# Kernel optimization log

Hardware: AMD Instinct MI355X
Metric: run time of the kernel (lower is better)

## Reference

```python
import jax, jax.numpy as jnp
import numpy as np

N_USERS = 100000
N_ITEMS = 50000
EMB_DIM = 64
N_EDGES = 1000000
N_HOPS = 3
EPS = 1e-12  # F.normalize default eps


def _l2_normalize(x):
    # F.normalize(x): x / max(||x||_2, eps) along dim=1
    norm = jnp.sqrt(jnp.sum(x * x, axis=1, keepdims=True))
    return x / jnp.maximum(norm, EPS)


def setup_inputs() -> dict:
    key = jax.random.key(0)
    k1, k2, k3, k4 = jax.random.split(key, 4)
    user_emb = jax.random.normal(k1, (N_USERS, EMB_DIM), dtype=jnp.float32)
    item_emb = jax.random.normal(k2, (N_ITEMS, EMB_DIM), dtype=jnp.float32)
    user_indices = jax.random.randint(k3, (N_EDGES,), 0, N_USERS, dtype=jnp.int32)
    item_indices = jax.random.randint(k4, (N_EDGES,), 0, N_ITEMS, dtype=jnp.int32)
    return {"user_emb": user_emb, "item_emb": item_emb,
            "user_indices": user_indices, "item_indices": item_indices}


def reference(user_emb, item_emb, user_indices, item_indices):
    # mess_dropout=False, node_dropout=False (deterministic reference)
    user_agg = user_emb
    item_agg = item_emb
    user_ui_emb = jnp.zeros_like(user_emb)
    item_ui_emb = jnp.zeros_like(item_emb)
    for _ in range(N_HOPS):
        # bipartite message passing: gather from opposite side, scatter_add to own side
        msg_to_users = item_agg[item_indices]            # [E, D]
        msg_to_items = user_agg[user_indices]            # [E, D]
        user_agg = jax.ops.segment_sum(msg_to_users, user_indices, num_segments=N_USERS)
        item_agg = jax.ops.segment_sum(msg_to_items, item_indices, num_segments=N_ITEMS)
        item_agg = _l2_normalize(item_agg)
        user_agg = _l2_normalize(user_agg)
        user_ui_emb = user_agg + user_ui_emb
        item_ui_emb = item_agg + item_ui_emb
    item_ui_emb = item_ui_emb + item_emb
    user_ui_emb = user_ui_emb + user_emb
    return (item_ui_emb, user_ui_emb)
```

## Files before the change

### kernel.cpp

```cpp
#include <hip/hip_runtime.h>

#define N_USERS 100000
#define N_ITEMS 50000
#define NROWS (N_USERS + N_ITEMS)
#define EMB 64
#define N_EDGES 1000000

#define SH_U 9
#define SH_I 8
#define NBUK 196
#define B1 256
#define CHUNK ((N_EDGES + B1 - 1) / B1)
#define HN (2 * NBUK * B1)
#define HTILE 4096
#define HTILES ((HN + HTILE - 1) / HTILE)
#define DBINS 64

typedef unsigned short u16;
typedef u16 us8 __attribute__((ext_vector_type(8)));
typedef u16 us4 __attribute__((ext_vector_type(4)));
typedef float f4 __attribute__((ext_vector_type(4)));

static __device__ __forceinline__ float bf2f(u16 h) {
    return __uint_as_float(((unsigned)h) << 16);
}
static __device__ __forceinline__ u16 f2bf(float f) {
    unsigned u = __float_as_uint(f);
    return (u16)((u + 0x7FFFu + ((u >> 16) & 1u)) >> 16);
}

static __device__ __forceinline__ int hphys(int L) {
    int sb = L >> 8;
    int blk = L & 255;
    return blk * (2 * NBUK) + sb;
}

__global__ void conv_kernel(const float* __restrict__ a, u16* __restrict__ b, int n4) {
    int t = blockIdx.x * blockDim.x + threadIdx.x;
    if (t >= n4) return;
    f4 v = ((const f4*)a)[t];
    us4 w;
    w.x = f2bf(v.x); w.y = f2bf(v.y); w.z = f2bf(v.z); w.w = f2bf(v.w);
    ((us4*)b)[t] = w;
}

__global__ void histA_kernel(const int* __restrict__ uidx, const int* __restrict__ iidx,
                             int* __restrict__ H) {
    __shared__ int hu[NBUK];
    __shared__ int hi[NBUK];
    int tid = threadIdx.x, blk = blockIdx.x;
    for (int b = tid; b < NBUK; b += 256) { hu[b] = 0; hi[b] = 0; }
    __syncthreads();
    int e0 = blk * CHUNK;
    int e1 = e0 + CHUNK; if (e1 > N_EDGES) e1 = N_EDGES;
    for (int e = e0 + tid; e < e1; e += 256) {
        atomicAdd(&hu[uidx[e] >> SH_U], 1);
        atomicAdd(&hi[iidx[e] >> SH_I], 1);
    }
    __syncthreads();
    int* Hb = H + blk * (2 * NBUK);
    for (int b = tid; b < NBUK; b += 256) {
        Hb[b] = hu[b];
        Hb[NBUK + b] = hi[b];
    }
}

__global__ void hscan_tile_kernel(const int* __restrict__ H, int* __restrict__ part) {
    int t = blockIdx.x, tid = threadIdx.x;
    int base = t * HTILE;
    int s = 0;
    for (int i = tid; i < HTILE; i += 256) {
        int L = base + i;
        if (L < HN) s += H[hphys(L)];
    }
    #pragma unroll
    for (int o = 32; o > 0; o >>= 1) s += __shfl_xor(s, o);
    __shared__ int wsum[4];
    if ((tid & 63) == 0) wsum[tid >> 6] = s;
    __syncthreads();
    if (tid == 0) part[t] = wsum[0] + wsum[1] + wsum[2] + wsum[3];
}

__global__ void hscan_write_kernel(const int* __restrict__ H, const int* __restrict__ part,
                                   int* __restrict__ HB) {
    int t = blockIdx.x, tid = threadIdx.x;
    int base = t * HTILE;

    __shared__ int lds[HTILE];
    for (int i = tid; i < HTILE; i += 256) {
        int L = base + i;
        lds[i] = (L < HN) ? H[hphys(L)] : 0;
    }
    __syncthreads();

    int pbase = 0;
    for (int p = 0; p < t; ++p) pbase += part[p];

    int tsum = 0;
    #pragma unroll
    for (int i = 0; i < 16; ++i) tsum += lds[tid * 16 + i];

    int lane = tid & 63, wid = tid >> 6;
    int x = tsum;
    #pragma unroll
    for (int o = 1; o < 64; o <<= 1) {
        int tt = __shfl_up(x, o);
        if (lane >= o) x += tt;
    }
    __shared__ int wsum[4];
    if (lane == 63) wsum[wid] = x;
    __syncthreads();
    int wbase = 0;
    for (int w = 0; w < wid; ++w) wbase += wsum[w];

    int run = pbase + wbase + x - tsum;
    #pragma unroll
    for (int i = 0; i < 16; ++i) {
        int L = base + tid * 16 + i;
        if (L < HN) HB[L] = run;
        run += lds[tid * 16 + i];
    }
}

__global__ void scatterA_kernel(const int* __restrict__ uidx, const int* __restrict__ iidx,
                                const int* __restrict__ HB, int* __restrict__ rec) {
    __shared__ int cu[NBUK];
    __shared__ int ci[NBUK];
    int tid = threadIdx.x, blk = blockIdx.x;
    for (int sb = tid; sb < 2 * NBUK; sb += 256) {
        int v = HB[sb * B1 + blk];
        if (sb < NBUK) cu[sb] = v; else ci[sb - NBUK] = v;
    }
    __syncthreads();
    int e0 = blk * CHUNK;
    int e1 = e0 + CHUNK; if (e1 > N_EDGES) e1 = N_EDGES;
    for (int e = e0 + tid; e < e1; e += 256) {
        int u = uidx[e];
        int i = iidx[e];
        int pu = atomicAdd(&cu[u >> SH_U], 1);
        rec[pu] = ((u & 511) << 16) | i;
        int pi = atomicAdd(&ci[i >> SH_I], 1);
        rec[pi] = ((i & 255) << 17) | u;
    }
}

__global__ void bucketB_kernel(const int* __restrict__ HB, const int* __restrict__ rec,
                               int* __restrict__ offs_u, int* __restrict__ offs_i,
                               int* __restrict__ list, int* __restrict__ perm) {
    int sb = blockIdx.x, tid = threadIdx.x;
    int side = (sb >= NBUK) ? 1 : 0;
    int b = sb - side * NBUK;
    int start = HB[sb * B1];
    int end = (sb == 2 * NBUK - 1) ? 2 * N_EDGES : HB[(sb + 1) * B1];
    int shift = side ? 17 : 16;
    int mask  = side ? 0x1FFFF : 0xFFFF;
    int nd    = side ? 256 : 512;
    int dbase = side ? (b << SH_I) : (b << SH_U);
    int n     = side ? N_ITEMS : N_USERS;
    int rel   = start - side * N_EDGES;
    int* offs = side ? offs_i : offs_u;

    __shared__ int cnt[512];
    __shared__ int scn[512];
    __shared__ int wsum[4];
    __shared__ int dh[DBINS];
    __shared__ int dsc[DBINS];
    if (tid < 256) { cnt[tid] = 0; cnt[256 + tid] = 0; }
    if (tid < DBINS) dh[tid] = 0;
    __syncthreads();

    for (int r = start + tid; r < end; r += 256)
        atomicAdd(&cnt[rec[r] >> shift], 1);
    __syncthreads();

    int a0 = cnt[2 * tid], a1 = cnt[2 * tid + 1];
    int s = a0 + a1;
    int lane = tid & 63, wid = tid >> 6;
    int x = s;
    #pragma unroll
    for (int o = 1; o < 64; o <<= 1) {
        int tt = __shfl_up(x, o);
        if (lane >= o) x += tt;
    }
    if (lane == 63) wsum[wid] = x;
    __syncthreads();
    int wbase = 0;
    for (int w = 0; w < wid; ++w) wbase += wsum[w];
    int excl = wbase + x - s;
    scn[2 * tid] = excl;
    scn[2 * tid + 1] = excl + a0;
    __syncthreads();

    for (int dl = tid; dl < nd; dl += 256) {
        int dg = dbase + dl;
        if (dg < n) offs[dg] = rel + scn[dl];
    }
    if (b == NBUK - 1 && tid == 0) offs[n] = (end - side * N_EDGES);
    __syncthreads();

    for (int r = start + tid; r < end; r += 256) {
        int v = rec[r];
        int dl = v >> shift;
        int pos = atomicAdd(&scn[dl], 1);
        list[start + pos] = (v & mask) << 7;
    }

    int nv = n - dbase; if (nv > nd) nv = nd;
    for (int dl = tid; dl < nv; dl += 256) {
        int d = cnt[dl]; if (d > DBINS - 1) d = DBINS - 1;
        atomicAdd(&dh[d], 1);
    }
    __syncthreads();
    if (tid < DBINS) {
        int v = dh[tid];
        int xx = v;
        #pragma unroll
        for (int o = 1; o < DBINS; o <<= 1) {
            int tt = __shfl_up(xx, o);
            if (tid >= o) xx += tt;
        }
        dsc[tid] = xx - v;
    }
    __syncthreads();
    if (tid < DBINS) dh[tid] = dsc[tid];
    __syncthreads();
    int pwbase = side ? (N_USERS + dbase) : dbase;
    for (int dl = tid; dl < nv; dl += 256) {
        int d = cnt[dl]; if (d > DBINS - 1) d = DBINS - 1;
        int p = atomicAdd(&dh[d], 1);
        perm[pwbase + p] = pwbase + dl;
    }
}

__global__ void gather_norm_v3(const u16* __restrict__ srcU,
                               const u16* __restrict__ srcI,
                               const int* __restrict__ offs_u, const int* __restrict__ list_u,
                               const int* __restrict__ offs_i, const int* __restrict__ list_i,
                               const int* __restrict__ perm,
                               u16* __restrict__ aggU, u16* __restrict__ aggI,
                               const u16* __restrict__ h0U, const u16* __restrict__ h0I,
                               const u16* __restrict__ h1U, const u16* __restrict__ h1I,
                               float* __restrict__ outU, float* __restrict__ outI,
                               const float* __restrict__ initU, const float* __restrict__ initI,
                               int final_hop) {
    int t = blockIdx.x * blockDim.x + threadIdx.x;
    int lane = t & 63;
    int grp = lane >> 3, sub = lane & 7;
    int slot = (t >> 6) * 8 + grp;

    int rid = (slot < NROWS) ? perm[slot] : -1;
    bool valid = rid >= 0;
    bool isU = valid && (rid < N_USERS);
    int rr = isU ? rid : rid - N_USERS;

    int beg = 0, deg = 0;
    if (valid) {
        const int* offs = isU ? offs_u : offs_i;
        beg = offs[rr];
        deg = offs[rr + 1] - beg;
    }
    const int* list = isU ? list_u : list_i;
    const u16* src  = isU ? srcU : srcI;
    const char* srcB = (const char*)src;
    unsigned suboff = (unsigned)(sub << 4);
    const int* lp = list + beg;

    int dmax = deg;
    dmax = max(dmax, __shfl_xor(dmax, 8));
    dmax = max(dmax, __shfl_xor(dmax, 16));
    dmax = max(dmax, __shfl_xor(dmax, 32));

    float acc[8] = {0.f, 0.f, 0.f, 0.f, 0.f, 0.f, 0.f, 0.f};

    #pragma unroll 8
    for (int e = 0; e < dmax; ++e) {
        if (e < deg) {
            unsigned jb = (unsigned)lp[e];
            us8 v = *(const us8*)(srcB + (jb + suboff));
            #pragma unroll
            for (int i = 0; i < 8; ++i) acc[i] += bf2f(v[i]);
        }
    }

    float q = 0.f;
    #pragma unroll
    for (int i = 0; i < 8; ++i) q += acc[i] * acc[i];
    q += __shfl_xor(q, 1);
    q += __shfl_xor(q, 2);
    q += __shfl_xor(q, 4);
    float inv = 1.f / fmaxf(sqrtf(q), 1e-12f);

    if (!valid) return;
    size_t ro = (size_t)rr * EMB + (sub << 3);

    if (!final_hop) {
        u16* agg = isU ? aggU : aggI;
        us8 w;
        #pragma unroll
        for (int i = 0; i < 8; ++i) w[i] = f2bf(acc[i] * inv);
        *(us8*)(agg + ro) = w;
    } else {
        const u16* h0 = isU ? h0U : h0I;
        const u16* h1 = isU ? h1U : h1I;
        const float* init = isU ? initU : initI;
        float* out = isU ? outU : outI;
        us8 a = *(const us8*)(h0 + ro);
        us8 b = *(const us8*)(h1 + ro);
        f4 i0 = *(const f4*)(init + ro);
        f4 i1 = *(const f4*)(init + ro + 4);
        f4 r0, r1;
        r0.x = i0.x + bf2f(a[0]) + bf2f(b[0]) + acc[0] * inv;
        r0.y = i0.y + bf2f(a[1]) + bf2f(b[1]) + acc[1] * inv;
        r0.z = i0.z + bf2f(a[2]) + bf2f(b[2]) + acc[2] * inv;
        r0.w = i0.w + bf2f(a[3]) + bf2f(b[3]) + acc[3] * inv;
        r1.x = i1.x + bf2f(a[4]) + bf2f(b[4]) + acc[4] * inv;
        r1.y = i1.y + bf2f(a[5]) + bf2f(b[5]) + acc[5] * inv;
        r1.z = i1.z + bf2f(a[6]) + bf2f(b[6]) + acc[6] * inv;
        r1.w = i1.w + bf2f(a[7]) + bf2f(b[7]) + acc[7] * inv;
        *(f4*)(out + ro)     = r0;
        *(f4*)(out + ro + 4) = r1;
    }
}

extern "C" void kernel_launch(void* const* d_in, const int* in_sizes, int n_in,
                              void* d_out, int out_size, void* d_ws, size_t ws_size,
                              hipStream_t stream) {
    const float* user_emb = (const float*)d_in[0];
    const float* item_emb = (const float*)d_in[1];
    const int*   uidx     = (const int*)d_in[2];
    const int*   iidx     = (const int*)d_in[3];

    float* out      = (float*)d_out;
    float* out_item = out;
    float* out_user = out + (size_t)N_ITEMS * EMB;

    u16* ws16    = (u16*)d_ws;
    u16* ua_bf   = ws16;
    u16* ub_bf   = ua_bf + (size_t)N_USERS * EMB;
    u16* ia_bf   = ub_bf + (size_t)N_USERS * EMB;
    u16* ib_bf   = ia_bf + (size_t)N_ITEMS * EMB;
    u16* uemb_bf = ib_bf + (size_t)N_ITEMS * EMB;
    u16* iemb_bf = uemb_bf + (size_t)N_USERS * EMB;
    int* rec     = (int*)(iemb_bf + (size_t)N_ITEMS * EMB);
    int* list    = rec + 2 * N_EDGES;
    int* list_u  = list;
    int* list_i  = list + N_EDGES;
    int* offs_u  = list + 2 * N_EDGES;
    int* offs_i  = offs_u + (N_USERS + 1);
    int* H       = offs_i + (N_ITEMS + 1);
    int* HB      = H + HN;
    int* part    = HB + HN;
    int* perm    = part + HTILES;

    conv_kernel<<<(N_USERS * EMB / 4 + 255) / 256, 256, 0, stream>>>(user_emb, uemb_bf, N_USERS * EMB / 4);
    conv_kernel<<<(N_ITEMS * EMB / 4 + 255) / 256, 256, 0, stream>>>(item_emb, iemb_bf, N_ITEMS * EMB / 4);

    histA_kernel<<<B1, 256, 0, stream>>>(uidx, iidx, H);
    hscan_tile_kernel<<<HTILES, 256, 0, stream>>>(H, part);
    hscan_write_kernel<<<HTILES, 256, 0, stream>>>(H, part, HB);
    scatterA_kernel<<<B1, 256, 0, stream>>>(uidx, iidx, HB, rec);
    bucketB_kernel<<<2 * NBUK, 256, 0, stream>>>(HB, rec, offs_u, offs_i, list, perm);

    const int gthreads = ((NROWS + 7) / 8) * 64;
    const int gblocks = (gthreads + 255) / 256;

    gather_norm_v3<<<gblocks, 256, 0, stream>>>(
        iemb_bf, uemb_bf, offs_u, list_u, offs_i, list_i, perm,
        ua_bf, ia_bf, nullptr, nullptr, nullptr, nullptr,
        nullptr, nullptr, nullptr, nullptr, 0);

    gather_norm_v3<<<gblocks, 256, 0, stream>>>(
        ia_bf, ua_bf, offs_u, list_u, offs_i, list_i, perm,
        ub_bf, ib_bf, nullptr, nullptr, nullptr, nullptr,
        nullptr, nullptr, nullptr, nullptr, 0);

    gather_norm_v3<<<gblocks, 256, 0, stream>>>(
        ib_bf, ub_bf, offs_u, list_u, offs_i, list_i, perm,
        nullptr, nullptr, ua_bf, ia_bf, ub_bf, ib_bf,
        out_user, out_item, user_emb, item_emb, 1);
}
```

Measured before the change: 239.2 us.

## Pack per-row descriptors, batch edge-index loads via shuffles, fuse conversion kernels

Replaces the separate perm and offset arrays with a packed int2 descriptor per sorted slot (begin, row id and degree). Each gather row needs one load instead of a dependent chain of perm then two offs reads. In the gather loop, each 8-lane group loads 8 edge indices at once and broadcasts them with shuffles, replacing per-edge scalar list loads. It also merges the two bf16 conversion launches into one and remaps block IDs in an XCD-interleaved pattern with a hardcoded grid of 4688. The risks are that degree is capped at 511 by the 9-bit packing, and the block-count constants are hardcoded.

After: 228.5 us. 1.05x faster.

```diff
diff --git a/kernel.cpp b/kernel.cpp
--- a/kernel.cpp
+++ b/kernel.cpp
@@ -35,13 +35,19 @@
     return blk * (2 * NBUK) + sb;
 }
 
-__global__ void conv_kernel(const float* __restrict__ a, u16* __restrict__ b, int n4) {
+__global__ void conv_kernel(const float* __restrict__ ua, u16* __restrict__ ub,
+                            const float* __restrict__ ia, u16* __restrict__ ib) {
+    const int un4 = N_USERS * EMB / 4;
+    const int in4 = N_ITEMS * EMB / 4;
     int t = blockIdx.x * blockDim.x + threadIdx.x;
-    if (t >= n4) return;
-    f4 v = ((const f4*)a)[t];
+    const float* a; u16* b; int idx;
+    if (t < un4) { a = ua; b = ub; idx = t; }
+    else if (t < un4 + in4) { a = ia; b = ib; idx = t - un4; }
+    else return;
+    f4 v = ((const f4*)a)[idx];
     us4 w;
     w.x = f2bf(v.x); w.y = f2bf(v.y); w.z = f2bf(v.z); w.w = f2bf(v.w);
-    ((us4*)b)[t] = w;
+    ((us4*)b)[idx] = w;
 }
 
 __global__ void histA_kernel(const int* __restrict__ uidx, const int* __restrict__ iidx,
@@ -145,8 +151,7 @@
 }
 
 __global__ void bucketB_kernel(const int* __restrict__ HB, const int* __restrict__ rec,
-                               int* __restrict__ offs_u, int* __restrict__ offs_i,
-                               int* __restrict__ list, int* __restrict__ perm) {
+                               int* __restrict__ list, int2* __restrict__ desc) {
     int sb = blockIdx.x, tid = threadIdx.x;
     int side = (sb >= NBUK) ? 1 : 0;
     int b = sb - side * NBUK;
@@ -157,8 +162,6 @@
     int nd    = side ? 256 : 512;
     int dbase = side ? (b << SH_I) : (b << SH_U);
     int n     = side ? N_ITEMS : N_USERS;
-    int rel   = start - side * N_EDGES;
-    int* offs = side ? offs_i : offs_u;
 
     __shared__ int cnt[512];
     __shared__ int scn[512];
@@ -191,19 +194,13 @@
     scn[2 * tid + 1] = excl + a0;
     __syncthreads();
 
-    for (int dl = tid; dl < nd; dl += 256) {
-        int dg = dbase + dl;
-        if (dg < n) offs[dg] = rel + scn[dl];
-    }
-    if (b == NBUK - 1 && tid == 0) offs[n] = (end - side * N_EDGES);
-    __syncthreads();
-
     for (int r = start + tid; r < end; r += 256) {
         int v = rec[r];
         int dl = v >> shift;
         int pos = atomicAdd(&scn[dl], 1);
         list[start + pos] = (v & mask) << 7;
     }
+    __syncthreads();
 
     int nv = n - dbase; if (nv > nd) nv = nd;
     for (int dl = tid; dl < nv; dl += 256) {
@@ -226,40 +223,44 @@
     __syncthreads();
     int pwbase = side ? (N_USERS + dbase) : dbase;
     for (int dl = tid; dl < nv; dl += 256) {
-        int d = cnt[dl]; if (d > DBINS - 1) d = DBINS - 1;
+        int deg = cnt[dl];
+        int d = deg; if (d > DBINS - 1) d = DBINS - 1;
         int p = atomicAdd(&dh[d], 1);
-        perm[pwbase + p] = pwbase + dl;
-    }
-}
-
-__global__ void gather_norm_v3(const u16* __restrict__ srcU,
+        int absBeg = start + scn[dl] - deg;
+        int rid = pwbase + dl;
+        desc[pwbase + p] = make_int2(absBeg, (rid << 9) | deg);
+    }
+}
+
+__global__ void gather_norm_v4(const u16* __restrict__ srcU,
                                const u16* __restrict__ srcI,
-                               const int* __restrict__ offs_u, const int* __restrict__ list_u,
-                               const int* __restrict__ offs_i, const int* __restrict__ list_i,
-                               const int* __restrict__ perm,
+                               const int* __restrict__ list,
+                               const int2* __restrict__ desc,
                                u16* __restrict__ aggU, u16* __restrict__ aggI,
                                const u16* __restrict__ h0U, const u16* __restrict__ h0I,
                                const u16* __restrict__ h1U, const u16* __restrict__ h1I,
                                float* __restrict__ outU, float* __restrict__ outI,
                                const float* __restrict__ initU, const float* __restrict__ initI,
                                int final_hop) {
-    int t = blockIdx.x * blockDim.x + threadIdx.x;
+    int bid = blockIdx.x;
+    int wg = (bid & 7) * 586 + (bid >> 3);
+
+    int t = wg * 256 + threadIdx.x;
     int lane = t & 63;
     int grp = lane >> 3, sub = lane & 7;
     int slot = (t >> 6) * 8 + grp;
 
-    int rid = (slot < NROWS) ? perm[slot] : -1;
-    bool valid = rid >= 0;
-    bool isU = valid && (rid < N_USERS);
+    int beg = 0, deg = 0, rid = 0;
+    bool valid = slot < NROWS;
+    if (valid) {
+        int2 d2 = desc[slot];
+        beg = d2.x;
+        deg = d2.y & 511;
+        rid = d2.y >> 9;
+    }
+    bool isU = rid < N_USERS;
     int rr = isU ? rid : rid - N_USERS;
 
-    int beg = 0, deg = 0;
-    if (valid) {
-        const int* offs = isU ? offs_u : offs_i;
-        beg = offs[rr];
-        deg = offs[rr + 1] - beg;
-    }
-    const int* list = isU ? list_u : list_i;
     const u16* src  = isU ? srcU : srcI;
     const char* srcB = (const char*)src;
     unsigned suboff = (unsigned)(sub << 4);
@@ -272,13 +273,19 @@
 
     float acc[8] = {0.f, 0.f, 0.f, 0.f, 0.f, 0.f, 0.f, 0.f};
 
-    #pragma unroll 8
-    for (int e = 0; e < dmax; ++e) {
-        if (e < deg) {
-            unsigned jb = (unsigned)lp[e];
-            us8 v = *(const us8*)(srcB + (jb + suboff));
-            #pragma unroll
-            for (int i = 0; i < 8; ++i) acc[i] += bf2f(v[i]);
+    int lbase = lane & 56;
+    int nbatch = (dmax + 7) >> 3;
+    for (int bch = 0; bch < nbatch; ++bch) {
+        int ebase = bch << 3;
+        int jb_l = lp[ebase + sub];
+        #pragma unroll
+        for (int e = 0; e < 8; ++e) {
+            if (ebase + e < deg) {
+                unsigned jb = (unsigned)__shfl(jb_l, lbase | e);
+                us8 v = *(const us8*)(srcB + (jb + suboff));
+                #pragma unroll
+                for (int i = 0; i < 8; ++i) acc[i] += bf2f(v[i]);
+            }
         }
     }
 
@@ -343,39 +350,33 @@
     u16* iemb_bf = uemb_bf + (size_t)N_USERS * EMB;
     int* rec     = (int*)(iemb_bf + (size_t)N_ITEMS * EMB);
     int* list    = rec + 2 * N_EDGES;
-    int* list_u  = list;
-    int* list_i  = list + N_EDGES;
-    int* offs_u  = list + 2 * N_EDGES;
-    int* offs_i  = offs_u + (N_USERS + 1);
-    int* H       = offs_i + (N_ITEMS + 1);
+    int* H       = list + 2 * N_EDGES + 16;
     int* HB      = H + HN;
     int* part    = HB + HN;
-    int* perm    = part + HTILES;
-
-    conv_kernel<<<(N_USERS * EMB / 4 + 255) / 256, 256, 0, stream>>>(user_emb, uemb_bf, N_USERS * EMB / 4);
-    conv_kernel<<<(N_ITEMS * EMB / 4 + 255) / 256, 256, 0, stream>>>(item_emb, iemb_bf, N_ITEMS * EMB / 4);
+    int2* desc   = (int2*)(part + HTILES + 1);
+
+    conv_kernel<<<(NROWS * EMB / 4 + 255) / 256, 256, 0, stream>>>(user_emb, uemb_bf, item_emb, iemb_bf);
 
     histA_kernel<<<B1, 256, 0, stream>>>(uidx, iidx, H);
     hscan_tile_kernel<<<HTILES, 256, 0, stream>>>(H, part);
     hscan_write_kernel<<<HTILES, 256, 0, stream>>>(H, part, HB);
     scatterA_kernel<<<B1, 256, 0, stream>>>(uidx, iidx, HB, rec);
-    bucketB_kernel<<<2 * NBUK, 256, 0, stream>>>(HB, rec, offs_u, offs_i, list, perm);
-
-    const int gthreads = ((NROWS + 7) / 8) * 64;
-    const int gblocks = (gthreads + 255) / 256;
-
-    gather_norm_v3<<<gblocks, 256, 0, stream>>>(
-        iemb_bf, uemb_bf, offs_u, list_u, offs_i, list_i, perm,
+    bucketB_kernel<<<2 * NBUK, 256, 0, stream>>>(HB, rec, list, desc);
+
+    const int gblocks = 4688;
+
+    gather_norm_v4<<<gblocks, 256, 0, stream>>>(
+        iemb_bf, uemb_bf, list, desc,
         ua_bf, ia_bf, nullptr, nullptr, nullptr, nullptr,
         nullptr, nullptr, nullptr, nullptr, 0);
 
-    gather_norm_v3<<<gblocks, 256, 0, stream>>>(
-        ia_bf, ua_bf, offs_u, list_u, offs_i, list_i, perm,
+    gather_norm_v4<<<gblocks, 256, 0, stream>>>(
+        ia_bf, ua_bf, list, desc,
         ub_bf, ib_bf, nullptr, nullptr, nullptr, nullptr,
         nullptr, nullptr, nullptr, nullptr, 0);
 
-    gather_norm_v3<<<gblocks, 256, 0, stream>>>(
-        ib_bf, ub_bf, offs_u, list_u, offs_i, list_i, perm,
+    gather_norm_v4<<<gblocks, 256, 0, stream>>>(
+        ib_bf, ub_bf, list, desc,
         nullptr, nullptr, ua_bf, ia_bf, ub_bf, ib_bf,
         out_user, out_item, user_emb, item_emb, 1);
 }
```
